# Optimization experiments

Hardware: AMD Instinct MI355X
Metric: run time of the kernel (lower is better)

The kernel has to match this reference:

```python
import jax, jax.numpy as jnp
import numpy as np

DIM = 768
NUM_HEADS = 12
HEAD_DIM = DIM // NUM_HEADS
SCALE = HEAD_DIM ** -0.5


def setup_inputs() -> dict:
    key = jax.random.key(0)
    ks = jax.random.split(key, 8)
    B, Nx, Ny = 4, 1024, 2048
    std = DIM ** -0.5
    return {
        "x": jax.random.normal(ks[0], (B, Nx, DIM), dtype=jnp.float32),
        "y": jax.random.normal(ks[1], (B, Ny, DIM), dtype=jnp.float32),
        "Wq": jax.random.normal(ks[2], (DIM, DIM), dtype=jnp.float32) * std,
        "Wk": jax.random.normal(ks[3], (DIM, DIM), dtype=jnp.float32) * std,
        "Wv": jax.random.normal(ks[4], (DIM, DIM), dtype=jnp.float32) * std,
        "Wproj": jax.random.normal(ks[5], (DIM, DIM), dtype=jnp.float32) * std,
        "bproj": jnp.zeros((DIM,), dtype=jnp.float32),
    }


def reference(x, y, Wq, Wk, Wv, Wproj, bproj):
    B, Nx, C = x.shape
    Ny = y.shape[1]
    H, D = NUM_HEADS, HEAD_DIM
    # Linear projections (torch nn.Linear: x @ W.T), then split heads -> [B,H,N,D]
    q = (x @ Wq.T).reshape(B, Nx, H, D).transpose(0, 2, 1, 3)
    k = (y @ Wk.T).reshape(B, Ny, H, D).transpose(0, 2, 1, 3)
    v = (y @ Wv.T).reshape(B, Ny, H, D).transpose(0, 2, 1, 3)
    # Manual attention: full [B,H,Nx,Ny] score matrix (faithful to source)
    attn = jnp.einsum("bhqd,bhkd->bhqk", q, k) * SCALE
    attn = jax.nn.softmax(attn, axis=-1)
    out = jnp.einsum("bhqk,bhkd->bhqd", attn, v)
    out = out.transpose(0, 2, 1, 3).reshape(B, Nx, C)
    return out @ Wproj.T + bproj
```

## Files before the change

### kernel.cpp

```cpp
#include <hip/hip_runtime.h>
#include <hip/hip_bf16.h>

typedef unsigned short u16;
typedef __attribute__((ext_vector_type(8))) short bf16x8;
typedef __attribute__((ext_vector_type(4))) float f32x4;
typedef __attribute__((ext_vector_type(16))) float f32x16;
typedef __attribute__((ext_vector_type(4))) unsigned u32x4;

#define MFMA(a, b, c) __builtin_amdgcn_mfma_f32_16x16x32_bf16(a, b, c, 0, 0, 0)
#define MFMA32(a, b, c) __builtin_amdgcn_mfma_f32_32x32x16_bf16(a, b, c, 0, 0, 0)

#define STAGE16(g, l) __builtin_amdgcn_global_load_lds( \
    (const __attribute__((address_space(1))) void*)(g),  \
    (__attribute__((address_space(3))) void*)(l), 16, 0, 0)

#define EXP2(x) __builtin_amdgcn_exp2f(x)

__device__ __forceinline__ u16 f2bf(float f) {
  union { float f; unsigned u; } v; v.f = f;
  return (u16)((v.u + 0x7fffu + ((v.u >> 16) & 1u)) >> 16);
}

__device__ __forceinline__ unsigned pack_bf2(float lo, float hi) {
  unsigned r;
  asm("v_cvt_pk_bf16_f32 %0, %1, %2" : "=v"(r) : "v"(lo), "v"(hi));
  return r;
}

__device__ __forceinline__ void pl32swap(unsigned &a, unsigned &b) {
  asm("v_permlane32_swap_b32 %0, %1" : "+v"(a), "+v"(b));
}

__global__ __launch_bounds__(256) void convert_all(
    const float* __restrict__ x, const float* __restrict__ y,
    const float* __restrict__ wq, const float* __restrict__ wk,
    const float* __restrict__ wv, const float* __restrict__ wp,
    u16* __restrict__ xb, u16* __restrict__ yb,
    u16* __restrict__ wqb, u16* __restrict__ wkb,
    u16* __restrict__ wvb, u16* __restrict__ wpb)
{
  constexpr int G0 = 4096 * 768 / 4;
  constexpr int G1 = G0 + 8192 * 768 / 4;
  constexpr int GW = 768 * 768 / 4;
  int g = blockIdx.x * 256 + threadIdx.x;
  const float* s; u16* d; int o;
  if      (g < G0)          { s = x;  d = xb;  o = g; }
  else if (g < G1)          { s = y;  d = yb;  o = g - G0; }
  else if (g < G1 + GW)     { s = wq; d = wqb; o = g - G1; }
  else if (g < G1 + 2*GW)   { s = wk; d = wkb; o = g - G1 - GW; }
  else if (g < G1 + 3*GW)   { s = wv; d = wvb; o = g - G1 - 2*GW; }
  else if (g < G1 + 4*GW)   { s = wp; d = wpb; o = g - G1 - 3*GW; }
  else return;
  float4 v = reinterpret_cast<const float4*>(s)[o];
  ushort4 r;
  r.x = f2bf(v.x); r.y = f2bf(v.y); r.z = f2bf(v.z); r.w = f2bf(v.w);
  reinterpret_cast<ushort4*>(d)[o] = r;
}

template <bool PROJ>
__global__ __launch_bounds__(256) void gemm_k(
    const u16* __restrict__ A0, const u16* __restrict__ A1,
    const u16* __restrict__ W0, const u16* __restrict__ W1,
    const u16* __restrict__ W2,
    u16* __restrict__ Qa, u16* __restrict__ Ka, u16* __restrict__ Vw,
    const float* __restrict__ bias, float* __restrict__ fout)
{
  __shared__ u16 sA[2][128 * 64];
  __shared__ u16 sB[2][128 * 64];

  const int nper = PROJ ? 24 : 120;
  int bid = (blockIdx.x & 7) * nper + (blockIdx.x >> 3);

  const u16 *A, *W;
  int mode, mt, nt;
  if (PROJ)           { mode = 3; A = A0; W = W0; mt = bid / 6;        nt = bid % 6; }
  else if (bid < 192) { mode = 0; A = A0; W = W0; mt = bid / 6;        nt = bid % 6; }
  else if (bid < 576) { mode = 1; A = A1; W = W1; mt = (bid-192) / 6;  nt = (bid-192) % 6; }
  else                { mode = 2; A = A1; W = W2; mt = (bid-576) / 6;  nt = (bid-576) % 6; }

  const int tid = threadIdx.x;
  const int w = tid >> 6, l = tid & 63;
  const int wm = w >> 1, wn = w & 1;
  const int g = l >> 4, m = l & 15;

  const int mbase = mt * 128, nbase = nt * 128;

  const int srow = l >> 3;
  const int schunk = ((l & 7) ^ srow) * 8;
  const u16* Ag = A + (size_t)(mbase + srow) * 768 + schunk;
  const u16* Wg = W + (size_t)(nbase + srow) * 768 + schunk;

  f32x4 acc[4][4] = {};

#pragma unroll
  for (int i = 0; i < 4; ++i) {
    const int ri = (i * 4 + w) * 8;
    STAGE16(Ag + (size_t)ri * 768, (char*)sA[0] + ri * 128);
    STAGE16(Wg + (size_t)ri * 768, (char*)sB[0] + ri * 128);
  }

  for (int kt = 0; kt < 12; ++kt) {
    __syncthreads();

    if (kt < 11) {
      const int ko = (kt + 1) * 64;
      const int nb = (kt + 1) & 1;
#pragma unroll
      for (int i = 0; i < 4; ++i) {
        const int ri = (i * 4 + w) * 8;
        STAGE16(Ag + (size_t)ri * 768 + ko, (char*)sA[nb] + ri * 128);
        STAGE16(Wg + (size_t)ri * 768 + ko, (char*)sB[nb] + ri * 128);
      }
    }

    const int cb = kt & 1;
    bf16x8 af[2][4], bfr[2][4];
#pragma unroll
    for (int c = 0; c < 2; ++c)
#pragma unroll
      for (int t = 0; t < 4; ++t) {
        const int ar = wm * 64 + t * 16 + m;
        const int br = wn * 64 + t * 16 + m;
        const int cp = ((c * 4 + g) ^ (l & 7)) * 16;
        af[c][t]  = *reinterpret_cast<const bf16x8*>((const char*)sA[cb] + ar * 128 + cp);
        bfr[c][t] = *reinterpret_cast<const bf16x8*>((const char*)sB[cb] + br * 128 + cp);
      }
#pragma unroll
    for (int c = 0; c < 2; ++c)
#pragma unroll
      for (int mi = 0; mi < 4; ++mi)
#pragma unroll
        for (int ni = 0; ni < 4; ++ni)
          acc[mi][ni] = MFMA(af[c][mi], bfr[c][ni], acc[mi][ni]);
  }

  const float QSCALE = 0.18033688011112042f;
  const int rowb = mbase + wm * 64 + g * 4;
  const int colb = nbase + wn * 64 + m;
#pragma unroll
  for (int mi = 0; mi < 4; ++mi) {
#pragma unroll
    for (int ni = 0; ni < 4; ++ni) {
      const int col = colb + ni * 16;
      const int h = col >> 6, d = col & 63;
      const int t_ = d >> 4, hh = (d >> 3) & 1, di = d & 7;
      const int fo = t_ * 512 + hh * 256 + di;
      if constexpr (PROJ) {
#pragma unroll
        for (int r = 0; r < 4; ++r) {
          const int row = rowb + mi * 16 + r;
          fout[(size_t)row * 768 + col] = acc[mi][ni][r] + bias[col];
        }
      } else {
        if (mode == 0) {
#pragma unroll
          for (int r = 0; r < 4; ++r) {
            const int row = rowb + mi * 16 + r;
            const int b_ = row >> 10, n = row & 1023;
            Qa[((size_t)(b_ * 12 + h) * 32 + (n >> 5)) * 2048 + fo + (n & 31) * 8] =
                f2bf(acc[mi][ni][r] * QSCALE);
          }
        } else if (mode == 1) {
#pragma unroll
          for (int r = 0; r < 4; ++r) {
            const int row = rowb + mi * 16 + r;
            const int b_ = row >> 11, n = row & 2047;
            Ka[(size_t)(b_ * 12 + h) * 131072 + (n >> 5) * 2048 + fo + (n & 31) * 8] =
                f2bf(acc[mi][ni][r]);
          }
        } else {
          const int row = rowb + mi * 16;
          const int b_ = row >> 11, n = row & 2047;
          ushort4 pk;
          pk.x = f2bf(acc[mi][ni][0]); pk.y = f2bf(acc[mi][ni][1]);
          pk.z = f2bf(acc[mi][ni][2]); pk.w = f2bf(acc[mi][ni][3]);
          *reinterpret_cast<ushort4*>(
              Vw + (size_t)(b_ * 12 + h) * 131072 + (n >> 3) * 512 + d * 8 + (n & 7)) = pk;
        }
      }
    }
  }
}

__global__ __launch_bounds__(128, 3) void attn_fwd(
    const u16* __restrict__ Qa, const u16* __restrict__ Ka,
    const u16* __restrict__ Vw, u16* __restrict__ AOb)
{
  __shared__ float cO[32 * 64];
  __shared__ float cL[2][32];

  const int bid = blockIdx.x;
  const int bh = bid % 48, qt = bid / 48;
  const int tid = threadIdx.x;
  const int w = tid >> 6, l = tid & 63;
  const int h = l >> 5, q = l & 31;

  const u16* qb = Qa + (size_t)(bh * 32 + qt) * 2048 + h * 256 + q * 8;
  bf16x8 qf[4];
#pragma unroll
  for (int t = 0; t < 4; ++t)
    qf[t] = *reinterpret_cast<const bf16x8*>(qb + t * 512);

  const u16* kb = Ka + (size_t)bh * 131072 + (size_t)w * 65536 + h * 256 + q * 8;
  const u16* vb = Vw + (size_t)bh * 131072 + (size_t)w * 65536 + h * 512 + q * 8;

  f32x16 o0 = {}, o1 = {};
  float lrun = 0.f;

#pragma unroll 1
  for (int kt2 = 0; kt2 < 8; ++kt2) {
    const u16* kpa = kb + (size_t)kt2 * 8192;
    const u16* vpa = vb + (size_t)kt2 * 8192;

    bf16x8 kfa0[4], kfa1[4], kfb0[4], kfb1[4], vfa0[4], vfa1[4];
#pragma unroll
    for (int t = 0; t < 4; ++t) {
      kfa0[t] = *reinterpret_cast<const bf16x8*>(kpa + t * 512);
      kfa1[t] = *reinterpret_cast<const bf16x8*>(kpa + 2048 + t * 512);
    }
#pragma unroll
    for (int t = 0; t < 4; ++t) {
      kfb0[t] = *reinterpret_cast<const bf16x8*>(kpa + 4096 + t * 512);
      kfb1[t] = *reinterpret_cast<const bf16x8*>(kpa + 6144 + t * 512);
    }
#pragma unroll
    for (int t = 0; t < 4; ++t) {
      vfa0[t] = *reinterpret_cast<const bf16x8*>(vpa + t * 1024);
      vfa1[t] = *reinterpret_cast<const bf16x8*>(vpa + t * 1024 + 256);
    }

    {
      f32x16 s0 = {}, s1 = {};
      __builtin_amdgcn_s_setprio(1);
#pragma unroll
      for (int t = 0; t < 4; ++t) {
        s0 = MFMA32(kfa0[t], qf[t], s0);
        s1 = MFMA32(kfa1[t], qf[t], s1);
      }
      __builtin_amdgcn_s_setprio(0);

      float p0[16], p1[16];
#pragma unroll
      for (int r = 0; r < 16; ++r) p0[r] = EXP2(s0[r]);
#pragma unroll
      for (int r = 0; r < 16; ++r) p1[r] = EXP2(s1[r]);

      float a8[8];
#pragma unroll
      for (int i = 0; i < 8; ++i)
        a8[i] = (p0[2*i] + p0[2*i+1]) + (p1[2*i] + p1[2*i+1]);
      float ts = ((a8[0]+a8[1]) + (a8[2]+a8[3])) + ((a8[4]+a8[5]) + (a8[6]+a8[7]));
      ts += __shfl_xor(ts, 32);
      lrun += ts;

      unsigned pk[2][4][2];
#pragma unroll
      for (int qd = 0; qd < 4; ++qd) {
        pk[0][qd][0] = pack_bf2(p0[4*qd+0], p0[4*qd+1]);
        pk[0][qd][1] = pack_bf2(p0[4*qd+2], p0[4*qd+3]);
        pk[1][qd][0] = pack_bf2(p1[4*qd+0], p1[4*qd+1]);
        pk[1][qd][1] = pack_bf2(p1[4*qd+2], p1[4*qd+3]);
      }

      __builtin_amdgcn_s_setprio(1);
#pragma unroll
      for (int t = 0; t < 4; ++t) {
        const int c = t >> 1, j0 = 2 * (t & 1);
        unsigned x0 = pk[c][j0][0], y0 = pk[c][j0 + 1][0];
        unsigned x1 = pk[c][j0][1], y1 = pk[c][j0 + 1][1];
        pl32swap(x0, y0);
        pl32swap(x1, y1);
        u32x4 fv; fv[0] = x0; fv[1] = x1; fv[2] = y0; fv[3] = y1;
        const bf16x8 af = __builtin_bit_cast(bf16x8, fv);
        o0 = MFMA32(af, vfa0[t], o0);
        o1 = MFMA32(af, vfa1[t], o1);
      }
      __builtin_amdgcn_s_setprio(0);
    }

    {
      bf16x8 vfb0[4], vfb1[4];
#pragma unroll
      for (int t = 0; t < 4; ++t) {
        vfb0[t] = *reinterpret_cast<const bf16x8*>(vpa + 4096 + t * 1024);
        vfb1[t] = *reinterpret_cast<const bf16x8*>(vpa + 4096 + t * 1024 + 256);
      }

      f32x16 s0 = {}, s1 = {};
      __builtin_amdgcn_s_setprio(1);
#pragma unroll
      for (int t = 0; t < 4; ++t) {
        s0 = MFMA32(kfb0[t], qf[t], s0);
        s1 = MFMA32(kfb1[t], qf[t], s1);
      }
      __builtin_amdgcn_s_setprio(0);

      float p0[16], p1[16];
#pragma unroll
      for (int r = 0; r < 16; ++r) p0[r] = EXP2(s0[r]);
#pragma unroll
      for (int r = 0; r < 16; ++r) p1[r] = EXP2(s1[r]);

      float a8[8];
#pragma unroll
      for (int i = 0; i < 8; ++i)
        a8[i] = (p0[2*i] + p0[2*i+1]) + (p1[2*i] + p1[2*i+1]);
      float ts = ((a8[0]+a8[1]) + (a8[2]+a8[3])) + ((a8[4]+a8[5]) + (a8[6]+a8[7]));
      ts += __shfl_xor(ts, 32);
      lrun += ts;

      unsigned pk[2][4][2];
#pragma unroll
      for (int qd = 0; qd < 4; ++qd) {
        pk[0][qd][0] = pack_bf2(p0[4*qd+0], p0[4*qd+1]);
        pk[0][qd][1] = pack_bf2(p0[4*qd+2], p0[4*qd+3]);
        pk[1][qd][0] = pack_bf2(p1[4*qd+0], p1[4*qd+1]);
        pk[1][qd][1] = pack_bf2(p1[4*qd+2], p1[4*qd+3]);
      }

      __builtin_amdgcn_s_setprio(1);
#pragma unroll
      for (int t = 0; t < 4; ++t) {
        const int c = t >> 1, j0 = 2 * (t & 1);
        unsigned x0 = pk[c][j0][0], y0 = pk[c][j0 + 1][0];
        unsigned x1 = pk[c][j0][1], y1 = pk[c][j0 + 1][1];
        pl32swap(x0, y0);
        pl32swap(x1, y1);
        u32x4 fv; fv[0] = x0; fv[1] = x1; fv[2] = y0; fv[3] = y1;
        const bf16x8 af = __builtin_bit_cast(bf16x8, fv);
        o0 = MFMA32(af, vfb0[t], o0);
        o1 = MFMA32(af, vfb1[t], o1);
      }
      __builtin_amdgcn_s_setprio(0);
    }
  }

  if (w == 1) {
    if (h == 0) cL[1][q] = lrun;
#pragma unroll
    for (int r = 0; r < 16; ++r) {
      const int crow = (r >> 2) * 8 + 4 * h + (r & 3);
      cO[crow * 64 + q]      = o0[r];
      cO[crow * 64 + 32 + q] = o1[r];
    }
  } else {
    if (h == 0) cL[0][q] = lrun;
  }
  __syncthreads();
  if (w == 0) {
    const int b_ = bh / 12, hd = bh % 12;
#pragma unroll
    for (int r = 0; r < 16; ++r) {
      const int crow = (r >> 2) * 8 + 4 * h + (r & 3);
      const float lt = cL[0][crow] + cL[1][crow];
      const float rl = 1.f / lt;
      const float ot0 = o0[r] + cO[crow * 64 + q];
      const float ot1 = o1[r] + cO[crow * 64 + 32 + q];
      u16* dst = AOb + ((size_t)b_ * 1024 + qt * 32 + crow) * 768 + hd * 64 + q;
      dst[0]  = f2bf(ot0 * rl);
      dst[32] = f2bf(ot1 * rl);
    }
  }
}

extern "C" void kernel_launch(void* const* d_in, const int* in_sizes, int n_in,
                              void* d_out, int out_size, void* d_ws, size_t ws_size,
                              hipStream_t stream)
{
  const float* x  = (const float*)d_in[0];
  const float* y  = (const float*)d_in[1];
  const float* wq = (const float*)d_in[2];
  const float* wk = (const float*)d_in[3];
  const float* wv = (const float*)d_in[4];
  const float* wp = (const float*)d_in[5];
  const float* bp = (const float*)d_in[6];
  float* out = (float*)d_out;

  char* ws = (char*)d_ws;
  u16* xb  = (u16*)ws; ws += (size_t)4096 * 768 * 2;
  u16* yb  = (u16*)ws; ws += (size_t)8192 * 768 * 2;
  u16* wqb = (u16*)ws; ws += (size_t)768 * 768 * 2;
  u16* wkb = (u16*)ws; ws += (size_t)768 * 768 * 2;
  u16* wvb = (u16*)ws; ws += (size_t)768 * 768 * 2;
  u16* wpb = (u16*)ws; ws += (size_t)768 * 768 * 2;
  u16* Qa  = (u16*)ws; ws += (size_t)4096 * 768 * 2;
  u16* Ka  = (u16*)ws; ws += (size_t)8192 * 768 * 2;
  u16* Vw  = (u16*)ws; ws += (size_t)8192 * 768 * 2;
  u16* AOb = (u16*)ws; ws += (size_t)4096 * 768 * 2;

  convert_all<<<11520, 256, 0, stream>>>(x, y, wq, wk, wv, wp,
                                         xb, yb, wqb, wkb, wvb, wpb);
  gemm_k<false><<<960, 256, 0, stream>>>(xb, yb, wqb, wkb, wvb,
                                         Qa, Ka, Vw, nullptr, nullptr);
  attn_fwd<<<1536, 128, 0, stream>>>(Qa, Ka, Vw, AOb);
  gemm_k<true><<<192, 256, 0, stream>>>(AOb, nullptr, wpb, nullptr, nullptr,
                                        nullptr, nullptr, nullptr, bp, out);
}
```

Measured before the change: 103.6 us.

## Process two query tiles per attention block to reuse K/V fragments

Each attention block now handles two 32-row query tiles instead of one and reuses every loaded K and V fragment for both, halving global K/V traffic per query. The grid shrinks from 1536 to 768 blocks and the key loop walks 16 smaller steps rather than 8 double steps. The cost is more live accumulators and registers per thread, the removal of the occupancy hint in launch bounds, doubled LDS for the cross-wave reduction, and fewer blocks to fill the GPU.

```diff
diff --git a/kernel.cpp b/kernel.cpp
--- a/kernel.cpp
+++ b/kernel.cpp
@@ -182,68 +182,76 @@
   }
 }
 
-__global__ __launch_bounds__(128, 3) void attn_fwd(
+__global__ __launch_bounds__(128) void attn_fwd(
     const u16* __restrict__ Qa, const u16* __restrict__ Ka,
     const u16* __restrict__ Vw, u16* __restrict__ AOb)
 {
-  __shared__ float cO[32 * 64];
-  __shared__ float cL[2][32];
+  __shared__ float cO[2][32 * 64];
+  __shared__ float cL[2][2][32];
 
   const int bid = blockIdx.x;
-  const int bh = bid % 48, qt = bid / 48;
+  const int bh = bid % 48, qp = bid / 48;
   const int tid = threadIdx.x;
   const int w = tid >> 6, l = tid & 63;
   const int h = l >> 5, q = l & 31;
 
-  const u16* qb = Qa + (size_t)(bh * 32 + qt) * 2048 + h * 256 + q * 8;
-  bf16x8 qf[4];
-#pragma unroll
-  for (int t = 0; t < 4; ++t)
-    qf[t] = *reinterpret_cast<const bf16x8*>(qb + t * 512);
+  const u16* qbA = Qa + (size_t)(bh * 32 + qp * 2) * 2048 + h * 256 + q * 8;
+  const u16* qbB = qbA + 2048;
+  bf16x8 qfA[4], qfB[4];
+#pragma unroll
+  for (int t = 0; t < 4; ++t) {
+    qfA[t] = *reinterpret_cast<const bf16x8*>(qbA + t * 512);
+    qfB[t] = *reinterpret_cast<const bf16x8*>(qbB + t * 512);
+  }
 
   const u16* kb = Ka + (size_t)bh * 131072 + (size_t)w * 65536 + h * 256 + q * 8;
   const u16* vb = Vw + (size_t)bh * 131072 + (size_t)w * 65536 + h * 512 + q * 8;
 
-  f32x16 o0 = {}, o1 = {};
-  float lrun = 0.f;
-
-#pragma unroll 1
-  for (int kt2 = 0; kt2 < 8; ++kt2) {
-    const u16* kpa = kb + (size_t)kt2 * 8192;
-    const u16* vpa = vb + (size_t)kt2 * 8192;
-
-    bf16x8 kfa0[4], kfa1[4], kfb0[4], kfb1[4], vfa0[4], vfa1[4];
+  f32x16 oA0 = {}, oA1 = {}, oB0 = {}, oB1 = {};
+  float lA = 0.f, lB = 0.f;
+
+  for (int kt = 0; kt < 16; ++kt) {
+    const u16* kp = kb + kt * 4096;
+    const u16* vp = vb + kt * 4096;
+
+    bf16x8 kf0[4], kf1[4];
 #pragma unroll
     for (int t = 0; t < 4; ++t) {
-      kfa0[t] = *reinterpret_cast<const bf16x8*>(kpa + t * 512);
-      kfa1[t] = *reinterpret_cast<const bf16x8*>(kpa + 2048 + t * 512);
-    }
+      kf0[t] = *reinterpret_cast<const bf16x8*>(kp + t * 512);
+      kf1[t] = *reinterpret_cast<const bf16x8*>(kp + 2048 + t * 512);
+    }
+
+    f32x16 sA0 = {}, sA1 = {};
+    __builtin_amdgcn_s_setprio(1);
 #pragma unroll
     for (int t = 0; t < 4; ++t) {
-      kfb0[t] = *reinterpret_cast<const bf16x8*>(kpa + 4096 + t * 512);
-      kfb1[t] = *reinterpret_cast<const bf16x8*>(kpa + 6144 + t * 512);
-    }
+      sA0 = MFMA32(kf0[t], qfA[t], sA0);
+      sA1 = MFMA32(kf1[t], qfA[t], sA1);
+    }
+    __builtin_amdgcn_s_setprio(0);
+
+    bf16x8 vf0[4], vf1[4];
 #pragma unroll
     for (int t = 0; t < 4; ++t) {
-      vfa0[t] = *reinterpret_cast<const bf16x8*>(vpa + t * 1024);
-      vfa1[t] = *reinterpret_cast<const bf16x8*>(vpa + t * 1024 + 256);
-    }
+      vf0[t] = *reinterpret_cast<const bf16x8*>(vp + t * 1024);
+      vf1[t] = *reinterpret_cast<const bf16x8*>(vp + t * 1024 + 256);
+    }
+
+    f32x16 sB0 = {}, sB1 = {};
+    __builtin_amdgcn_s_setprio(1);
+#pragma unroll
+    for (int t = 0; t < 4; ++t) {
+      sB0 = MFMA32(kf0[t], qfB[t], sB0);
+      sB1 = MFMA32(kf1[t], qfB[t], sB1);
+    }
+    __builtin_amdgcn_s_setprio(0);
 
     {
-      f32x16 s0 = {}, s1 = {};
-      __builtin_amdgcn_s_setprio(1);
-#pragma unroll
-      for (int t = 0; t < 4; ++t) {
-        s0 = MFMA32(kfa0[t], qf[t], s0);
-        s1 = MFMA32(kfa1[t], qf[t], s1);
-      }
-      __builtin_amdgcn_s_setprio(0);
-
       float p0[16], p1[16];
 #pragma unroll
-      for (int r = 0; r < 16; ++r) p0[r] = EXP2(s0[r]);
-#pragma unroll
-      for (int r = 0; r < 16; ++r) p1[r] = EXP2(s1[r]);
+      for (int r = 0; r < 16; ++r) p0[r] = EXP2(sA0[r]);
+#pragma unroll
+      for (int r = 0; r < 16; ++r) p1[r] = EXP2(sA1[r]);
 
       float a8[8];
 #pragma unroll
@@ -251,7 +259,7 @@
         a8[i] = (p0[2*i] + p0[2*i+1]) + (p1[2*i] + p1[2*i+1]);
       float ts = ((a8[0]+a8[1]) + (a8[2]+a8[3])) + ((a8[4]+a8[5]) + (a8[6]+a8[7]));
       ts += __shfl_xor(ts, 32);
-      lrun += ts;
+      lA += ts;
 
       unsigned pk[2][4][2];
 #pragma unroll
@@ -272,34 +280,18 @@
         pl32swap(x1, y1);
         u32x4 fv; fv[0] = x0; fv[1] = x1; fv[2] = y0; fv[3] = y1;
         const bf16x8 af = __builtin_bit_cast(bf16x8, fv);
-        o0 = MFMA32(af, vfa0[t], o0);
-        o1 = MFMA32(af, vfa1[t], o1);
+        oA0 = MFMA32(af, vf0[t], oA0);
+        oA1 = MFMA32(af, vf1[t], oA1);
       }
       __builtin_amdgcn_s_setprio(0);
     }
 
     {
-      bf16x8 vfb0[4], vfb1[4];
-#pragma unroll
-      for (int t = 0; t < 4; ++t) {
-        vfb0[t] = *reinterpret_cast<const bf16x8*>(vpa + 4096 + t * 1024);
-        vfb1[t] = *reinterpret_cast<const bf16x8*>(vpa + 4096 + t * 1024 + 256);
-      }
-
-      f32x16 s0 = {}, s1 = {};
-      __builtin_amdgcn_s_setprio(1);
-#pragma unroll
-      for (int t = 0; t < 4; ++t) {
-        s0 = MFMA32(kfb0[t], qf[t], s0);
-        s1 = MFMA32(kfb1[t], qf[t], s1);
-      }
-      __builtin_amdgcn_s_setprio(0);
-
       float p0[16], p1[16];
 #pragma unroll
-      for (int r = 0; r < 16; ++r) p0[r] = EXP2(s0[r]);
-#pragma unroll
-      for (int r = 0; r < 16; ++r) p1[r] = EXP2(s1[r]);
+      for (int r = 0; r < 16; ++r) p0[r] = EXP2(sB0[r]);
+#pragma unroll
+      for (int r = 0; r < 16; ++r) p1[r] = EXP2(sB1[r]);
 
       float a8[8];
 #pragma unroll
@@ -307,7 +299,7 @@
         a8[i] = (p0[2*i] + p0[2*i+1]) + (p1[2*i] + p1[2*i+1]);
       float ts = ((a8[0]+a8[1]) + (a8[2]+a8[3])) + ((a8[4]+a8[5]) + (a8[6]+a8[7]));
       ts += __shfl_xor(ts, 32);
-      lrun += ts;
+      lB += ts;
 
       unsigned pk[2][4][2];
 #pragma unroll
@@ -328,23 +320,23 @@
         pl32swap(x1, y1);
         u32x4 fv; fv[0] = x0; fv[1] = x1; fv[2] = y0; fv[3] = y1;
         const bf16x8 af = __builtin_bit_cast(bf16x8, fv);
-        o0 = MFMA32(af, vfb0[t], o0);
-        o1 = MFMA32(af, vfb1[t], o1);
+        oB0 = MFMA32(af, vf0[t], oB0);
+        oB1 = MFMA32(af, vf1[t], oB1);
       }
       __builtin_amdgcn_s_setprio(0);
     }
   }
 
+  if (h == 0) { cL[w][0][q] = lA; cL[w][1][q] = lB; }
   if (w == 1) {
-    if (h == 0) cL[1][q] = lrun;
 #pragma unroll
     for (int r = 0; r < 16; ++r) {
       const int crow = (r >> 2) * 8 + 4 * h + (r & 3);
-      cO[crow * 64 + q]      = o0[r];
-      cO[crow * 64 + 32 + q] = o1[r];
-    }
-  } else {
-    if (h == 0) cL[0][q] = lrun;
+      cO[0][crow * 64 + q]      = oA0[r];
+      cO[0][crow * 64 + 32 + q] = oA1[r];
+      cO[1][crow * 64 + q]      = oB0[r];
+      cO[1][crow * 64 + 32 + q] = oB1[r];
+    }
   }
   __syncthreads();
   if (w == 0) {
@@ -352,13 +344,18 @@
 #pragma unroll
     for (int r = 0; r < 16; ++r) {
       const int crow = (r >> 2) * 8 + 4 * h + (r & 3);
-      const float lt = cL[0][crow] + cL[1][crow];
-      const float rl = 1.f / lt;
-      const float ot0 = o0[r] + cO[crow * 64 + q];
-      const float ot1 = o1[r] + cO[crow * 64 + 32 + q];
-      u16* dst = AOb + ((size_t)b_ * 1024 + qt * 32 + crow) * 768 + hd * 64 + q;
-      dst[0]  = f2bf(ot0 * rl);
-      dst[32] = f2bf(ot1 * rl);
+      const float rlA = 1.f / (cL[0][0][crow] + cL[1][0][crow]);
+      const float otA0 = oA0[r] + cO[0][crow * 64 + q];
+      const float otA1 = oA1[r] + cO[0][crow * 64 + 32 + q];
+      u16* dstA = AOb + ((size_t)b_ * 1024 + (qp * 2) * 32 + crow) * 768 + hd * 64 + q;
+      dstA[0]  = f2bf(otA0 * rlA);
+      dstA[32] = f2bf(otA1 * rlA);
+      const float rlB = 1.f / (cL[0][1][crow] + cL[1][1][crow]);
+      const float otB0 = oB0[r] + cO[1][crow * 64 + q];
+      const float otB1 = oB1[r] + cO[1][crow * 64 + 32 + q];
+      u16* dstB = AOb + ((size_t)b_ * 1024 + (qp * 2 + 1) * 32 + crow) * 768 + hd * 64 + q;
+      dstB[0]  = f2bf(otB0 * rlB);
+      dstB[32] = f2bf(otB1 * rlB);
     }
   }
 }
@@ -392,7 +389,7 @@
                                          xb, yb, wqb, wkb, wvb, wpb);
   gemm_k<false><<<960, 256, 0, stream>>>(xb, yb, wqb, wkb, wvb,
                                          Qa, Ka, Vw, nullptr, nullptr);
-  attn_fwd<<<1536, 128, 0, stream>>>(Qa, Ka, Vw, AOb);
+  attn_fwd<<<768, 128, 0, stream>>>(Qa, Ka, Vw, AOb);
   gemm_k<true><<<192, 256, 0, stream>>>(AOb, nullptr, wpb, nullptr, nullptr,
                                         nullptr, nullptr, nullptr, bp, out);
 }
```

New measurement: 110.2 us. 1.06x slower.
